# Performance work log

Hardware: AMD Instinct MI355X
Metric: run time of the kernel (lower is better)

The kernel has to match this reference:

```python
import jax, jax.numpy as jnp
import numpy as np

B, N = 16, 65536
N_BOUND = 50           # n_boundaries, linear spacing in [0, 1]
EMBD_LEN = N_BOUND + 1 # 51 learned bucket vectors
EMBD_DIM = 50
OUT_DIM = 50
HID = 2 * EMBD_DIM + 1 # 101, MLP width


def _xavier(key, shape):
    fan_in, fan_out = shape[1], shape[0]
    std = (2.0 / (fan_in + fan_out)) ** 0.5
    return jax.random.normal(key, shape, jnp.float32) * std


def setup_inputs() -> dict:
    key = jax.random.key(0)
    ks = jax.random.split(key, 6)
    x = jax.random.normal(ks[0], (B, N, 1), jnp.float32)
    boundaries = jnp.linspace(0.0, 1.0, N_BOUND).astype(jnp.float32)
    embd = _xavier(ks[1], (EMBD_LEN, EMBD_DIM))
    embd_oob = _xavier(ks[2], (2, OUT_DIM))
    w1 = _xavier(ks[3], (HID, HID))
    b1 = jnp.zeros((HID,), jnp.float32)
    w2 = _xavier(ks[4], (OUT_DIM, HID))
    b2 = jnp.zeros((OUT_DIM,), jnp.float32)
    return {"x": x, "boundaries": boundaries, "embd": embd,
            "embd_oob": embd_oob, "w1": w1, "b1": b1, "w2": w2, "b2": b2}


def reference(x, boundaries, embd, embd_oob, w1, b1, w2, b2):
    xv = x[..., 0]                                   # (B, N)
    # torch.searchsorted default (right=False) == jnp side='left'
    idx = jnp.searchsorted(boundaries, xv)           # in [0, N_BOUND]
    padded = jnp.concatenate([boundaries[:1], boundaries, boundaries[-1:]])  # (N_BOUND+2,)
    lo = padded[idx]
    hi = padded[idx + 1]
    rng = hi - lo
    # rng==0 only where idx is out-of-range (0 or EMBD_LEN-1); those outputs
    # are overwritten below, so guard the division to stay NaN-free.
    dist = (xv - lo) / jnp.where(rng == 0, 1.0, rng)  # (B, N)
    # in-range bucket indices live in [1, EMBD_LEN-2]; clip so idx+1 gather is safe
    ic = jnp.clip(idx, 1, EMBD_LEN - 2)
    feat = jnp.concatenate([embd[ic], embd[ic + 1], dist[..., None]], axis=-1)  # (B, N, 2*EMBD_DIM+1)
    h = jax.nn.gelu(feat @ w1.T + b1, approximate=False)  # torch nn.GELU = exact erf
    mlp_out = h @ w2.T + b2                           # (B, N, OUT_DIM)
    below = (idx == 0)[..., None]
    above = (idx == EMBD_LEN - 1)[..., None]
    out = jnp.where(below, embd_oob[0], jnp.where(above, embd_oob[1], mlp_out))
    return out
```

## Files before the change

### kernel.cpp

```cpp
#include <hip/hip_runtime.h>
#include <math.h>

#define NB        50
#define ED        50
#define OD        50
#define HID       101
#define K         129
#define NBUCKET   49
#define NSAMP     (NBUCKET * K)
#define ROWSTRIDE 52
#define NP        (16 * 65536)
#define CHUNK     17
#define NCHUNK    8

typedef float    f32x2 __attribute__((ext_vector_type(2)));
typedef _Float16 f16x2 __attribute__((ext_vector_type(2)));

__device__ __align__(16) _Float16 g_table[NSAMP * ROWSTRIDE];

__global__ __launch_bounds__(256) void build_table(
    const float* __restrict__ embd,
    const float* __restrict__ w1,
    const float* __restrict__ b1,
    const float* __restrict__ w2,
    const float* __restrict__ b2)
{
    const int blk = blockIdx.x;
    const int t   = threadIdx.x;
    const int bu  = blk >> 3;
    const int ch  = blk & 7;

    __shared__ float w2s[OD * 104];
    __shared__ float hs[CHUNK * 104];
    __shared__ float zc[224];

    for (int i = t; i < OD * HID; i += 256) {
        const int o = i / HID, j = i - o * HID;
        w2s[o * 104 + j] = w2[i];
    }
    if (t < HID) {
        const float* __restrict__ w1r = w1 + t * HID;
        const float* __restrict__ ea  = embd + (bu + 1) * ED;
        float acc = b1[t];
        #pragma unroll 10
        for (int kk = 0; kk < ED; kk++)
            acc = fmaf(ea[kk], w1r[kk], fmaf(ea[ED + kk], w1r[ED + kk], acc));
        zc[t]       = acc;
        zc[112 + t] = w1r[2 * ED];
    }
    __syncthreads();

    #pragma unroll
    for (int si = 0; si < CHUNK; si++) {
        const int k = ch * CHUNK + si;
        if (t < HID && k < K) {
            const float dist = (float)k * (1.0f / 128.0f);
            const float z = fmaf(dist, zc[112 + t], zc[t]);
            hs[si * 104 + t] = 0.5f * z * (1.0f + erff(z * 0.70710678118654752f));
        }
    }
    __syncthreads();

    for (int d = t; d < CHUNK * OD; d += 256) {
        const int si = d / OD, o = d - si * OD;
        const int k = ch * CHUNK + si;
        if (k >= K) continue;
        float acc = b2[o];
        const float4* __restrict__ h4 = (const float4*)(hs  + si * 104);
        const float4* __restrict__ w4 = (const float4*)(w2s + o  * 104);
        #pragma unroll
        for (int jj = 0; jj < 25; jj++) {
            const float4 hh = h4[jj], ww = w4[jj];
            acc = fmaf(hh.x, ww.x, acc);
            acc = fmaf(hh.y, ww.y, acc);
            acc = fmaf(hh.z, ww.z, acc);
            acc = fmaf(hh.w, ww.w, acc);
        }
        acc = fmaf(hs[si * 104 + 100], w2s[o * 104 + 100], acc);
        g_table[(bu * K + k) * ROWSTRIDE + o] = (_Float16)acc;
    }
}

__global__ __launch_bounds__(256) void embed_main(
    const float* __restrict__ x,
    const float* __restrict__ boundaries,
    const float* __restrict__ embd_oob,
    float* __restrict__ out)
{
    __shared__ float sB[NB];
    __shared__ f32x2 sTail[50];
    __shared__ int2  s_rows[256];
    __shared__ float s_frac[256];
    const int t = threadIdx.x;
    if (t < NB) sB[t] = boundaries[t];
    if (t < 2 * OD) ((float*)sTail)[t] = embd_oob[t];
    __syncthreads();

    const int p = blockIdx.x * 256 + t;
    const float xv = __builtin_nontemporal_load(&x[p]);

    int   r0, r1;
    float frac = 0.0f;
    if (xv <= sB[0]) {
        r0 = -1;  r1 = -1;
    } else if (xv > sB[NB - 1]) {
        r0 = -26; r1 = -26;
    } else {
        int j = (int)(xv * 49.0f);
        if (j > 48) j = 48;
        const int idx = (xv > sB[j]) ? ((xv > sB[j + 1]) ? j + 2 : j + 1) : j;
        const float lo = sB[idx - 1];
        const float hi = sB[idx];
        const float dist = (xv - lo) / (hi - lo);
        const float tt = dist * 128.0f;
        int k0 = (int)tt;
        if (k0 > 127) k0 = 127;
        frac = tt - (float)k0;
        const int row = (idx - 1) * K + k0;
        r0 = row * 26; r1 = r0 + 26;
    }
    s_rows[t] = make_int2(r0, r1);
    s_frac[t] = frac;
    __syncthreads();

    const f16x2* __restrict__ tabh = (const f16x2*)g_table;
    f32x2* __restrict__ o2 = (f32x2*)out + (size_t)blockIdx.x * 6400;

    #pragma unroll
    for (int i = 0; i < 25; i++) {
        const int e  = i * 256 + t;
        const int pt = e / 25;
        const int c2 = e - pt * 25;
        const int2  rr = s_rows[pt];
        f32x2 r;
        if (rr.x >= 0) {
            const float fr = s_frac[pt];
            const f16x2 a = tabh[rr.x + c2];
            const f16x2 b = tabh[rr.y + c2];
            const float ax = (float)a.x, ay = (float)a.y;
            r.x = fmaf(fr, (float)b.x - ax, ax);
            r.y = fmaf(fr, (float)b.y - ay, ay);
        } else {
            r = sTail[c2 - rr.x - 1];
        }
        __builtin_nontemporal_store(r, &o2[e]);
    }
}

extern "C" void kernel_launch(void* const* d_in, const int* in_sizes, int n_in,
                              void* d_out, int out_size, void* d_ws, size_t ws_size,
                              hipStream_t stream) {
    const float* x    = (const float*)d_in[0];
    const float* bnd  = (const float*)d_in[1];
    const float* embd = (const float*)d_in[2];
    const float* oob  = (const float*)d_in[3];
    const float* w1   = (const float*)d_in[4];
    const float* b1   = (const float*)d_in[5];
    const float* w2   = (const float*)d_in[6];
    const float* b2   = (const float*)d_in[7];
    float* out = (float*)d_out;

    build_table<<<NBUCKET * NCHUNK, 256, 0, stream>>>(embd, w1, b1, w2, b2);
    embed_main<<<NP / 256, 256, 0, stream>>>(x, bnd, oob, out);
}
```

Baseline: 246.0 us.

## Stage w1 in shared memory, pack per-point data, drop nontemporal loads/stores

The table-build kernel now copies all of w1 into shared memory, unioned with the w2 and hidden buffers, before the first-layer dot products. Those dot products then read rows from LDS instead of strided global memory. The main kernel packs row offsets and fraction into one int4 per point so each output element needs a single LDS read. It also replaces nontemporal loads and stores with ordinary ones, which changes cache behaviour on the large output write.

```diff
diff --git a/kernel.cpp b/kernel.cpp
--- a/kernel.cpp
+++ b/kernel.cpp
@@ -30,25 +30,31 @@
     const int bu  = blk >> 3;
     const int ch  = blk & 7;
 
-    __shared__ float w2s[OD * 104];
-    __shared__ float hs[CHUNK * 104];
+    __shared__ union U {
+        float w1s[HID * HID];
+        struct { float w2s[OD * 104]; float hs[CHUNK * 104]; } p;
+    } u;
     __shared__ float zc[224];
+
+    for (int i = t; i < HID * HID; i += 256) u.w1s[i] = w1[i];
+    __syncthreads();
+
+    if (t < HID) {
+        const float* __restrict__ r  = u.w1s + t * HID;
+        const float* __restrict__ ea = embd + (bu + 1) * ED;
+        float acc = b1[t];
+        #pragma unroll 10
+        for (int kk = 0; kk < ED; kk++)
+            acc = fmaf(ea[kk], r[kk], fmaf(ea[ED + kk], r[ED + kk], acc));
+        zc[t]       = acc;
+        zc[112 + t] = r[2 * ED];
+    }
+    __syncthreads();
 
     for (int i = t; i < OD * HID; i += 256) {
         const int o = i / HID, j = i - o * HID;
-        w2s[o * 104 + j] = w2[i];
+        u.p.w2s[o * 104 + j] = w2[i];
     }
-    if (t < HID) {
-        const float* __restrict__ w1r = w1 + t * HID;
-        const float* __restrict__ ea  = embd + (bu + 1) * ED;
-        float acc = b1[t];
-        #pragma unroll 10
-        for (int kk = 0; kk < ED; kk++)
-            acc = fmaf(ea[kk], w1r[kk], fmaf(ea[ED + kk], w1r[ED + kk], acc));
-        zc[t]       = acc;
-        zc[112 + t] = w1r[2 * ED];
-    }
-    __syncthreads();
 
     #pragma unroll
     for (int si = 0; si < CHUNK; si++) {
@@ -56,7 +62,7 @@
         if (t < HID && k < K) {
             const float dist = (float)k * (1.0f / 128.0f);
             const float z = fmaf(dist, zc[112 + t], zc[t]);
-            hs[si * 104 + t] = 0.5f * z * (1.0f + erff(z * 0.70710678118654752f));
+            u.p.hs[si * 104 + t] = 0.5f * z * (1.0f + erff(z * 0.70710678118654752f));
         }
     }
     __syncthreads();
@@ -66,8 +72,8 @@
         const int k = ch * CHUNK + si;
         if (k >= K) continue;
         float acc = b2[o];
-        const float4* __restrict__ h4 = (const float4*)(hs  + si * 104);
-        const float4* __restrict__ w4 = (const float4*)(w2s + o  * 104);
+        const float4* __restrict__ h4 = (const float4*)(u.p.hs  + si * 104);
+        const float4* __restrict__ w4 = (const float4*)(u.p.w2s + o  * 104);
         #pragma unroll
         for (int jj = 0; jj < 25; jj++) {
             const float4 hh = h4[jj], ww = w4[jj];
@@ -76,7 +82,7 @@
             acc = fmaf(hh.z, ww.z, acc);
             acc = fmaf(hh.w, ww.w, acc);
         }
-        acc = fmaf(hs[si * 104 + 100], w2s[o * 104 + 100], acc);
+        acc = fmaf(u.p.hs[si * 104 + 100], u.p.w2s[o * 104 + 100], acc);
         g_table[(bu * K + k) * ROWSTRIDE + o] = (_Float16)acc;
     }
 }
@@ -89,15 +95,14 @@
 {
     __shared__ float sB[NB];
     __shared__ f32x2 sTail[50];
-    __shared__ int2  s_rows[256];
-    __shared__ float s_frac[256];
+    __shared__ int4  s_pk[256];
     const int t = threadIdx.x;
     if (t < NB) sB[t] = boundaries[t];
     if (t < 2 * OD) ((float*)sTail)[t] = embd_oob[t];
     __syncthreads();
 
     const int p = blockIdx.x * 256 + t;
-    const float xv = __builtin_nontemporal_load(&x[p]);
+    const float xv = x[p];
 
     int   r0, r1;
     float frac = 0.0f;
@@ -119,8 +124,7 @@
         const int row = (idx - 1) * K + k0;
         r0 = row * 26; r1 = r0 + 26;
     }
-    s_rows[t] = make_int2(r0, r1);
-    s_frac[t] = frac;
+    s_pk[t] = make_int4(r0, r1, __float_as_int(frac), 0);
     __syncthreads();
 
     const f16x2* __restrict__ tabh = (const f16x2*)g_table;
@@ -131,19 +135,19 @@
         const int e  = i * 256 + t;
         const int pt = e / 25;
         const int c2 = e - pt * 25;
-        const int2  rr = s_rows[pt];
+        const int4 pk = s_pk[pt];
         f32x2 r;
-        if (rr.x >= 0) {
-            const float fr = s_frac[pt];
-            const f16x2 a = tabh[rr.x + c2];
-            const f16x2 b = tabh[rr.y + c2];
+        if (pk.x >= 0) {
+            const float fr = __int_as_float(pk.z);
+            const f16x2 a = tabh[pk.x + c2];
+            const f16x2 b = tabh[pk.y + c2];
             const float ax = (float)a.x, ay = (float)a.y;
             r.x = fmaf(fr, (float)b.x - ax, ax);
             r.y = fmaf(fr, (float)b.y - ay, ay);
         } else {
-            r = sTail[c2 - rr.x - 1];
+            r = sTail[c2 - pk.x - 1];
         }
-        __builtin_nontemporal_store(r, &o2[e]);
+        o2[e] = r;
     }
 }
 
```

Result: faster. 237.9 us (-3.3%).
